# Kernel optimization log

Measured on AMD Instinct MI355X. Metric: run time of the kernel, lower is better.

## Reference

```python
import jax, jax.numpy as jnp
import numpy as np

B, C, H, W = 2, 512, 64, 64
HEADS, DHEAD = 8, 64
HID = HEADS * DHEAD  # 512
GROUPS = 32
EPS = 1e-5


def setup_inputs() -> dict:
    key = jax.random.key(0)
    ks = jax.random.split(key, 10)
    w_scale = 0.02
    return {
        "x": jax.random.normal(ks[0], (B, C, H, W), dtype=jnp.float32),
        "gamma": jnp.ones((C,), dtype=jnp.float32),
        "beta": jnp.zeros((C,), dtype=jnp.float32),
        "wq": jax.random.normal(ks[1], (HID, C), dtype=jnp.float32) * w_scale,
        "bq": jax.random.normal(ks[2], (HID,), dtype=jnp.float32) * w_scale,
        "wk": jax.random.normal(ks[3], (HID, C), dtype=jnp.float32) * w_scale,
        "bk": jax.random.normal(ks[4], (HID,), dtype=jnp.float32) * w_scale,
        "wv": jax.random.normal(ks[5], (HID, C), dtype=jnp.float32) * w_scale,
        "bv": jax.random.normal(ks[6], (HID,), dtype=jnp.float32) * w_scale,
        "wo": jax.random.normal(ks[7], (C, HID), dtype=jnp.float32) * w_scale,
        "bo": jax.random.normal(ks[8], (C,), dtype=jnp.float32) * w_scale,
    }


def _group_norm(x, gamma, beta):
    b, c, h, w = x.shape
    xg = x.reshape(b, GROUPS, c // GROUPS, h * w)
    mu = jnp.mean(xg, axis=(2, 3), keepdims=True)
    var = jnp.var(xg, axis=(2, 3), keepdims=True)
    xn = (xg - mu) * jax.lax.rsqrt(var + EPS)
    xn = xn.reshape(b, c, h, w)
    return xn * gamma[None, :, None, None] + beta[None, :, None, None]


def reference(x, gamma, beta, wq, bq, wk, bk, wv, bv, wo, bo):
    b, c, h, w = x.shape
    n = h * w
    # norm + flatten spatial; embedding=None -> self-attention on normed x
    xn = _group_norm(x, gamma, beta).reshape(b, c, n)
    # 1x1 Conv1d projections == channel matmuls
    q = jnp.einsum('oc,bcn->bon', wq, xn) + bq[None, :, None]
    k = jnp.einsum('oc,bcn->bon', wk, xn) + bk[None, :, None]
    v = jnp.einsum('oc,bcn->bon', wv, xn) + bv[None, :, None]
    scale = DHEAD ** (-0.25)  # applied to BOTH q and k, as in source
    qh = q.reshape(b, HEADS, DHEAD, n) * scale
    kh = k.reshape(b, HEADS, DHEAD, n) * scale
    vh = v.reshape(b, HEADS, DHEAD, n)
    # full NxN attention (the materialized score matrix targeted for kernel work)
    attn = jax.nn.softmax(jnp.einsum('bhdi,bhdj->bhij', qh, kh), axis=-1)
    out = jnp.einsum('bhij,bhdj->bhdi', attn, vh).reshape(b, HID, n)
    out = jnp.einsum('oc,bcn->bon', wo, out) + bo[None, :, None]
    out = out.reshape(b, c, h, w)
    return x + out  # in_channels == out_channels -> residual
```

## Files before the change

kernel.cpp:

```cpp
#include <hip/hip_runtime.h>
#include <math.h>

#define BB      2
#define CC      512
#define NN_TOK  4096
#define HEADS   8
#define DHEAD   64
#define HID     512
#define GROUPS  32
#define CPG     (CC / GROUPS)
#define EPS     1e-5f

typedef __bf16 bf16x8 __attribute__((ext_vector_type(8)));
typedef float  f32x4  __attribute__((ext_vector_type(4)));
typedef float  f32x16 __attribute__((ext_vector_type(16)));
typedef int    i32x8  __attribute__((ext_vector_type(8)));

static __device__ __forceinline__ unsigned short f2bf(float f) {
  __bf16 h = (__bf16)f;
  return __builtin_bit_cast(unsigned short, h);
}
static __device__ __forceinline__ float bf2f(unsigned short u) {
  unsigned v = (unsigned)u << 16;
  return __builtin_bit_cast(float, v);
}
static __device__ __forceinline__ unsigned pk_fp8x4(float a, float b, float c, float d) {
  int lo = __builtin_amdgcn_cvt_pk_fp8_f32(a, b, 0, false);
  return (unsigned)__builtin_amdgcn_cvt_pk_fp8_f32(c, d, lo, true);
}
static __device__ __forceinline__ unsigned char f2fp8(float a) {
  return (unsigned char)(__builtin_amdgcn_cvt_pk_fp8_f32(a, a, 0, false) & 0xff);
}
static __device__ __forceinline__ i32x8 ld_frag32(const unsigned char* p) {
  union { i32x8 v; long l[4]; } u;
  u.l[0] = *(const long*)(p + 0);
  u.l[1] = *(const long*)(p + 8);
  u.l[2] = *(const long*)(p + 16);
  u.l[3] = *(const long*)(p + 24);
  return u.v;
}
#define SC_ONE 0x7F7F7F7F
#define QKV_WS 32.0f
#define QKV_WS_INV 0.03125f
#define WO_WS 16.0f
#define WO_WS_INV 0.0625f

__global__ __launch_bounds__(256) void gn_stats_wconv_kernel(
    const float* __restrict__ x, float2* __restrict__ part,
    const float* __restrict__ wq, const float* __restrict__ wk,
    const float* __restrict__ wv, const float* __restrict__ wo,
    unsigned char* __restrict__ wq8, unsigned char* __restrict__ wk8,
    unsigned char* __restrict__ wv8, unsigned char* __restrict__ wo8) {
  int blk = blockIdx.x;
  int t = threadIdx.x;
  {
    int wsel = blk >> 6;
    int off = (blk & 63) * 4096 + t * 16;
    const float* s = (wsel == 0) ? wq : (wsel == 1) ? wk : (wsel == 2) ? wv : wo;
    unsigned char* d = (wsel == 0) ? wq8 : (wsel == 1) ? wk8 : (wsel == 2) ? wv8 : wo8;
    float sc = (wsel < 3) ? QKV_WS : WO_WS;
    #pragma unroll
    for (int i = 0; i < 4; ++i) {
      float4 a = *(const float4*)&s[off + i * 4];
      *(unsigned*)&d[off + i * 4] =
          pk_fp8x4(a.x * sc, a.y * sc, a.z * sc, a.w * sc);
    }
  }
  const float4* __restrict__ x4 = (const float4*)(x + (size_t)blk * 16384);
  float s = 0.f, ss = 0.f;
  #pragma unroll
  for (int i = 0; i < 16; ++i) {
    float4 v = x4[t + i * 256];
    s  += v.x + v.y + v.z + v.w;
    ss += v.x * v.x + v.y * v.y + v.z * v.z + v.w * v.w;
  }
  #pragma unroll
  for (int off = 32; off >= 1; off >>= 1) {
    s  += __shfl_down(s, off, 64);
    ss += __shfl_down(ss, off, 64);
  }
  __shared__ float rs[4], rss[4];
  int wid = t >> 6, lane = t & 63;
  if (lane == 0) { rs[wid] = s; rss[wid] = ss; }
  __syncthreads();
  if (t == 0) {
    float2 o;
    o.x = rs[0] + rs[1] + rs[2] + rs[3];
    o.y = rss[0] + rss[1] + rss[2] + rss[3];
    part[blk] = o;
  }
}

__global__ __launch_bounds__(256) void gn_norm_t_kernel(
    const float* __restrict__ x, const float* __restrict__ gamma,
    const float* __restrict__ beta, const float2* __restrict__ part,
    unsigned char* __restrict__ xnT8) {
  __shared__ __align__(16) unsigned short lds[64 * 72];
  __shared__ float mu4[4], rs4[4];
  int b = blockIdx.z;
  int t0 = blockIdx.x * 64, c0 = blockIdx.y * 64;
  int t = threadIdx.x;
  if (t < 4) {
    int g = (c0 >> 4) + t;
    int gi = b * GROUPS + g;
    float2 p0 = part[gi * 4 + 0], p1 = part[gi * 4 + 1];
    float2 p2 = part[gi * 4 + 2], p3 = part[gi * 4 + 3];
    float S = p0.x + p1.x + p2.x + p3.x;
    float SS = p0.y + p1.y + p2.y + p3.y;
    const float inv_n = 1.0f / (float)(CPG * NN_TOK);
    float mu = S * inv_n;
    float var = SS * inv_n - mu * mu;
    mu4[t] = mu;
    rs4[t] = rsqrtf(var + EPS);
  }
  __syncthreads();
  const float* __restrict__ xb = x + (size_t)b * CC * NN_TOK;
  #pragma unroll
  for (int i = 0; i < 4; ++i) {
    int f = t + i * 256;
    int row = f >> 4, c16 = f & 15;
    int c = c0 + row;
    float ga = gamma[c] * rs4[row >> 4];
    float be = beta[c] - mu4[row >> 4] * ga;
    float4 v = *(const float4*)&xb[(size_t)c * NN_TOK + t0 + c16 * 4];
    ushort4 pk;
    pk.x = f2bf(v.x * ga + be); pk.y = f2bf(v.y * ga + be);
    pk.z = f2bf(v.z * ga + be); pk.w = f2bf(v.w * ga + be);
    *(ushort4*)&lds[row * 72 + c16 * 4] = pk;
  }
  __syncthreads();
  unsigned char* __restrict__ ob = xnT8 + (size_t)b * NN_TOK * CC;
  #pragma unroll
  for (int i = 0; i < 2; ++i) {
    int f = t + i * 256;
    int row = f >> 3, ch = f & 7;
    float v0 = bf2f(lds[(ch * 8 + 0) * 72 + row]);
    float v1 = bf2f(lds[(ch * 8 + 1) * 72 + row]);
    float v2 = bf2f(lds[(ch * 8 + 2) * 72 + row]);
    float v3 = bf2f(lds[(ch * 8 + 3) * 72 + row]);
    float v4 = bf2f(lds[(ch * 8 + 4) * 72 + row]);
    float v5 = bf2f(lds[(ch * 8 + 5) * 72 + row]);
    float v6 = bf2f(lds[(ch * 8 + 6) * 72 + row]);
    float v7 = bf2f(lds[(ch * 8 + 7) * 72 + row]);
    unsigned lo = pk_fp8x4(v0, v1, v2, v3);
    unsigned hi = pk_fp8x4(v4, v5, v6, v7);
    *(uint2*)&ob[(size_t)(t0 + row) * CC + c0 + ch * 8] = make_uint2(lo, hi);
  }
}

__global__ __launch_bounds__(256, 3) void qkv_gemm_kernel(
    const unsigned char* __restrict__ xnT8,
    const unsigned char* __restrict__ wq8, const unsigned char* __restrict__ wk8,
    const unsigned char* __restrict__ wv8,
    const float* __restrict__ bq, const float* __restrict__ bk,
    const float* __restrict__ bv,
    unsigned char* __restrict__ qT8, unsigned char* __restrict__ kT8,
    unsigned char* __restrict__ vB8) {
  __shared__ __align__(16) unsigned char AB[2][2][128 * 72];
  int b = blockIdx.z;
  int y = blockIdx.y;
  int which = y >> 2, yl = y & 3;
  const unsigned char* __restrict__ W =
      (which == 0) ? wq8 : (which == 1) ? wk8 : wv8;
  const float* __restrict__ bias = (which == 0) ? bq : (which == 1) ? bk : bv;
  int m0 = yl * 128;
  int n0 = blockIdx.x * 128;
  const unsigned char* __restrict__ Bsrc = xnT8 + (size_t)b * NN_TOK * CC;
  int t = threadIdx.x, w = t >> 6, lane = t & 63;
  int wm = (w >> 1) * 64, wn = (w & 1) * 64;
  int l31 = lane & 31, q1h = lane >> 5;

  int sr0 = t >> 2, sr1 = (t + 256) >> 2, sch = t & 3;
  const unsigned char* Wa0 = &W[(size_t)(m0 + sr0) * CC + sch * 16];
  const unsigned char* Wa1 = &W[(size_t)(m0 + sr1) * CC + sch * 16];
  const unsigned char* Bb0 = &Bsrc[(size_t)(n0 + sr0) * CC + sch * 16];
  const unsigned char* Bb1 = &Bsrc[(size_t)(n0 + sr1) * CC + sch * 16];
  uint4 ra0 = *(const uint4*)(Wa0);
  uint4 ra1 = *(const uint4*)(Wa1);
  uint4 rb0 = *(const uint4*)(Bb0);
  uint4 rb1 = *(const uint4*)(Bb1);

  const f32x16 z16 = {0,0,0,0,0,0,0,0,0,0,0,0,0,0,0,0};
  f32x16 acc[2][2];
  #pragma unroll
  for (int mt = 0; mt < 2; ++mt)
    #pragma unroll
    for (int nt = 0; nt < 2; ++nt) acc[mt][nt] = z16;

  int cur = 0;
  for (int kc = 0; kc < CC; kc += 64) {
    __syncthreads();
    {
      unsigned char* As = AB[cur][0];
      unsigned char* Bs = AB[cur][1];
      unsigned char* ad0 = &As[sr0 * 72 + sch * 16];
      *(uint2*)ad0 = make_uint2(ra0.x, ra0.y);
      *(uint2*)(ad0 + 8) = make_uint2(ra0.z, ra0.w);
      unsigned char* ad1 = &As[sr1 * 72 + sch * 16];
      *(uint2*)ad1 = make_uint2(ra1.x, ra1.y);
      *(uint2*)(ad1 + 8) = make_uint2(ra1.z, ra1.w);
      unsigned char* bd0 = &Bs[sr0 * 72 + sch * 16];
      *(uint2*)bd0 = make_uint2(rb0.x, rb0.y);
      *(uint2*)(bd0 + 8) = make_uint2(rb0.z, rb0.w);
      unsigned char* bd1 = &Bs[sr1 * 72 + sch * 16];
      *(uint2*)bd1 = make_uint2(rb1.x, rb1.y);
      *(uint2*)(bd1 + 8) = make_uint2(rb1.z, rb1.w);
    }
    if (kc + 64 < CC) {
      ra0 = *(const uint4*)(Wa0 + kc + 64);
      ra1 = *(const uint4*)(Wa1 + kc + 64);
      rb0 = *(const uint4*)(Bb0 + kc + 64);
      rb1 = *(const uint4*)(Bb1 + kc + 64);
    }
    __syncthreads();
    const unsigned char* As = AB[cur][0];
    const unsigned char* Bs = AB[cur][1];
    i32x8 af[2], bfm[2];
    #pragma unroll
    for (int i = 0; i < 2; ++i) {
      af[i]  = ld_frag32(&As[(wm + i * 32 + l31) * 72 + q1h * 32]);
      bfm[i] = ld_frag32(&Bs[(wn + i * 32 + l31) * 72 + q1h * 32]);
    }
    #pragma unroll
    for (int mt = 0; mt < 2; ++mt)
      #pragma unroll
      for (int nt = 0; nt < 2; ++nt)
        acc[mt][nt] = __builtin_amdgcn_mfma_scale_f32_32x32x64_f8f6f4(
            af[mt], bfm[nt], acc[mt][nt], 0, 0, 0, SC_ONE, 0, SC_ONE);
    cur ^= 1;
  }
  __syncthreads();

  if (which < 2) {
    const float sc = (which == 0) ? 0.18033688011112043f : 1.0f;
    unsigned char* __restrict__ dstT = (which == 0) ? qT8 : kT8;
    unsigned char* buf = (unsigned char*)AB + w * 2560;
    int h = (m0 + wm) >> 6;
    const size_t hbase = (size_t)(b * HEADS + h) * NN_TOK;
    #pragma unroll
    for (int p = 0; p < 2; ++p) {
      #pragma unroll
      for (int mt = 0; mt < 2; ++mt) {
        #pragma unroll
        for (int g = 0; g < 4; ++g) {
          float4 bv4 = *(const float4*)&bias[m0 + wm + mt * 32 + g * 8 + q1h * 4];
          f32x16 a = acc[mt][p];
          unsigned pk = pk_fp8x4((a[4 * g + 0] * QKV_WS_INV + bv4.x) * sc,
                                 (a[4 * g + 1] * QKV_WS_INV + bv4.y) * sc,
                                 (a[4 * g + 2] * QKV_WS_INV + bv4.z) * sc,
                                 (a[4 * g + 3] * QKV_WS_INV + bv4.w) * sc);
          *(unsigned*)&buf[l31 * 80 + mt * 32 + g * 8 + q1h * 4] = pk;
        }
      }
      #pragma unroll
      for (int it = 0; it < 2; ++it) {
        int idx = it * 64 + lane;
        int row = idx >> 2, ch = idx & 3;
        int tok = n0 + wn + p * 32 + row;
        *(uint4*)&dstT[(hbase + tok) * DHEAD + ch * 16] =
            *(const uint4*)&buf[row * 80 + ch * 16];
      }
      __syncthreads();
    }
  } else {
    unsigned char* __restrict__ dst = vB8 + (size_t)b * HID * NN_TOK;
    #pragma unroll
    for (int mt = 0; mt < 2; ++mt) {
      #pragma unroll
      for (int g = 0; g < 4; ++g) {
        float4 bv4 = *(const float4*)&bias[m0 + wm + mt * 32 + g * 8 + q1h * 4];
        float bvr[4] = {bv4.x, bv4.y, bv4.z, bv4.w};
        #pragma unroll
        for (int nt = 0; nt < 2; ++nt) {
          int tok = n0 + wn + nt * 32 + l31;
          #pragma unroll
          for (int r = 0; r < 4; ++r) {
            int m = m0 + wm + mt * 32 + g * 8 + q1h * 4 + r;
            dst[(size_t)m * NN_TOK + tok] =
                f2fp8(acc[mt][nt][4 * g + r] * QKV_WS_INV + bvr[r]);
          }
        }
      }
    }
  }
}

__global__ __launch_bounds__(256) void outproj_kernel(
    const unsigned char* __restrict__ aoT8, const unsigned char* __restrict__ wo8,
    const float* __restrict__ bo, const float* __restrict__ x,
    float* __restrict__ out) {
  __shared__ __align__(16) unsigned char As8[2][128 * 80];
  __shared__ __align__(16) unsigned char Bs8[2][64 * 80];
  int b = blockIdx.z;
  int m0 = blockIdx.y * 128;
  int n0 = blockIdx.x * 64;
  const unsigned char* __restrict__ Bsrc = aoT8 + (size_t)b * NN_TOK * HID;
  int t = threadIdx.x, w = t >> 6, lane = t & 63;
  int wm = (w & 1) * 64, wn = (w >> 1) * 32;
  int l31 = lane & 31, q1h = lane >> 5;

  int ar0 = t >> 2, ar1 = (t + 256) >> 2, ach = t & 3;
  const unsigned char* pa0 = &wo8[(size_t)(m0 + ar0) * HID + ach * 16];
  const unsigned char* pa1 = &wo8[(size_t)(m0 + ar1) * HID + ach * 16];
  const unsigned char* pb  = &Bsrc[(size_t)(n0 + ar0) * HID + ach * 16];
  uint4 ra0 = *(const uint4*)(pa0);
  uint4 ra1 = *(const uint4*)(pa1);
  uint4 rb  = *(const uint4*)(pb);

  const f32x16 z16 = {0,0,0,0,0,0,0,0,0,0,0,0,0,0,0,0};
  f32x16 acc[2];
  acc[0] = z16; acc[1] = z16;

  int cur = 0;
  for (int kc = 0; kc < HID; kc += 64) {
    __syncthreads();
    *(uint4*)&As8[cur][ar0 * 80 + ach * 16] = ra0;
    *(uint4*)&As8[cur][ar1 * 80 + ach * 16] = ra1;
    *(uint4*)&Bs8[cur][ar0 * 80 + ach * 16] = rb;
    if (kc + 64 < HID) {
      ra0 = *(const uint4*)(pa0 + kc + 64);
      ra1 = *(const uint4*)(pa1 + kc + 64);
      rb  = *(const uint4*)(pb + kc + 64);
    }
    __syncthreads();
    i32x8 bfm = ld_frag32(&Bs8[cur][(wn + l31) * 80 + q1h * 32]);
    #pragma unroll
    for (int mt = 0; mt < 2; ++mt) {
      i32x8 af = ld_frag32(&As8[cur][(wm + mt * 32 + l31) * 80 + q1h * 32]);
      acc[mt] = __builtin_amdgcn_mfma_scale_f32_32x32x64_f8f6f4(
          af, bfm, acc[mt], 0, 0, 0, SC_ONE, 0, SC_ONE);
    }
    cur ^= 1;
  }

  const float* __restrict__ xb = x + (size_t)b * CC * NN_TOK;
  float* __restrict__ ob = out + (size_t)b * CC * NN_TOK;
  int tok = n0 + wn + l31;
  #pragma unroll
  for (int mt = 0; mt < 2; ++mt) {
    #pragma unroll
    for (int g = 0; g < 4; ++g) {
      float4 bv4 = *(const float4*)&bo[m0 + wm + mt * 32 + g * 8 + q1h * 4];
      float bvr[4] = {bv4.x, bv4.y, bv4.z, bv4.w};
      #pragma unroll
      for (int r = 0; r < 4; ++r) {
        int m = m0 + wm + mt * 32 + g * 8 + q1h * 4 + r;
        size_t off = (size_t)m * NN_TOK + tok;
        ob[off] = acc[mt][4 * g + r] * WO_WS_INV + bvr[r] + xb[off];
      }
    }
  }
}

__global__ __launch_bounds__(512, 4) void attn_mfma_kernel(
    const unsigned char* __restrict__ qT8, const unsigned char* __restrict__ kT8,
    const unsigned char* __restrict__ vv8, unsigned char* __restrict__ aoT8) {
  __shared__ __align__(16) unsigned char kvs[2 * 18432];
  __shared__ __align__(16) unsigned char st8[4 * 32 * 80];
  __shared__ float lbuf[128];
  int bh = blockIdx.y;
  int b = bh >> 3, h = bh & 7;
  int i0 = blockIdx.x * 128;
  const size_t hb = (size_t)bh * NN_TOK;
  const unsigned char* __restrict__ qtg = qT8 + hb * DHEAD;
  const unsigned char* __restrict__ ktg = kT8 + hb * DHEAD;
  const unsigned char* __restrict__ vg  = vv8 + hb * DHEAD;
  int t = threadIdx.x;
  int w = t >> 6, lane = t & 63, l31 = lane & 31, q1h = lane >> 5;
  int strip = w & 3, parity = w >> 2;
  int iw = i0 + strip * 32;

  const unsigned char* qrow = qtg + (size_t)(iw + l31) * DHEAD + q1h * 32;
  uint4 qv0 = *(const uint4*)(qrow);
  uint4 qv1 = *(const uint4*)(qrow + 16);
  i32x8 qf = {(int)qv0.x, (int)qv0.y, (int)qv0.z, (int)qv0.w,
              (int)qv1.x, (int)qv1.y, (int)qv1.z, (int)qv1.w};
  i32x8 ones;
  #pragma unroll
  for (int i = 0; i < 8; ++i) ones[i] = 0x38383838;

  int jr = t >> 2, ch = t & 3;
  int ktile = jr >> 6, krow = jr & 63;
  int vtile = t >> 8, vrr = (t >> 2) & 63, vch = t & 3;
  const unsigned char* kga = &ktg[(size_t)jr * DHEAD + ch * 16];
  const unsigned char* vga = &vg[(size_t)vrr * NN_TOK + vtile * 64 + vch * 16];
  int kldso = ktile * 4608 + krow * 72 + ch * 16;
  int vldso = 9216 + vtile * 4608 + vrr * 72 + vch * 16;

  uint4 kx = *(const uint4*)(kga);
  uint4 vx = *(const uint4*)(vga);

  const f32x16 z16 = {0,0,0,0,0,0,0,0,0,0,0,0,0,0,0,0};
  f32x16 o0 = z16, o1 = z16, lacc = z16;

  int cur = 0;
  for (int rt = 0; rt < NN_TOK / 128; ++rt) {
    __syncthreads();
    unsigned char* kb = kvs + cur * 18432;
    {
      unsigned char* kd = kb + kldso;
      *(uint2*)kd = make_uint2(kx.x, kx.y);
      *(uint2*)(kd + 8) = make_uint2(kx.z, kx.w);
      unsigned char* vd = kb + vldso;
      *(uint2*)vd = make_uint2(vx.x, vx.y);
      *(uint2*)(vd + 8) = make_uint2(vx.z, vx.w);
    }
    if (rt + 1 < NN_TOK / 128) {
      kx = *(const uint4*)(kga + (size_t)(rt + 1) * 128 * DHEAD);
      vx = *(const uint4*)(vga + (rt + 1) * 128);
    }
    __syncthreads();
    const unsigned char* ksw = kb + parity * 4608;
    const unsigned char* vsw = kb + 9216 + parity * 4608;

    i32x8 ka0 = ld_frag32(&ksw[l31 * 72 + q1h * 32]);
    i32x8 ka1 = ld_frag32(&ksw[(32 + l31) * 72 + q1h * 32]);
    f32x16 s0 = __builtin_amdgcn_mfma_scale_f32_32x32x64_f8f6f4(
        ka0, qf, z16, 0, 0, 0, SC_ONE, 0, SC_ONE);
    f32x16 s1 = __builtin_amdgcn_mfma_scale_f32_32x32x64_f8f6f4(
        ka1, qf, z16, 0, 0, 0, SC_ONE, 0, SC_ONE);

    unsigned pk4[8];
    #pragma unroll
    for (int g = 0; g < 4; ++g) {
      float p0 = __builtin_amdgcn_exp2f(s0[4 * g + 0]);
      float p1 = __builtin_amdgcn_exp2f(s0[4 * g + 1]);
      float p2 = __builtin_amdgcn_exp2f(s0[4 * g + 2]);
      float p3 = __builtin_amdgcn_exp2f(s0[4 * g + 3]);
      pk4[g] = pk_fp8x4(p0, p1, p2, p3);
    }
    #pragma unroll
    for (int g = 0; g < 4; ++g) {
      float p0 = __builtin_amdgcn_exp2f(s1[4 * g + 0]);
      float p1 = __builtin_amdgcn_exp2f(s1[4 * g + 1]);
      float p2 = __builtin_amdgcn_exp2f(s1[4 * g + 2]);
      float p3 = __builtin_amdgcn_exp2f(s1[4 * g + 3]);
      pk4[4 + g] = pk_fp8x4(p0, p1, p2, p3);
    }

    i32x8 pb;
    #pragma unroll
    for (int g = 0; g < 4; ++g) {
      unsigned send = q1h ? pk4[g] : pk4[4 + g];
      unsigned got = (unsigned)__shfl_xor((int)send, 32);
      pb[2 * g]     = (int)(q1h ? got : pk4[g]);
      pb[2 * g + 1] = (int)(q1h ? pk4[4 + g] : got);
    }

    i32x8 va0 = ld_frag32(&vsw[l31 * 72 + q1h * 32]);
    i32x8 va1 = ld_frag32(&vsw[(32 + l31) * 72 + q1h * 32]);
    o0 = __builtin_amdgcn_mfma_scale_f32_32x32x64_f8f6f4(
        va0, pb, o0, 0, 0, 0, SC_ONE, 0, SC_ONE);
    o1 = __builtin_amdgcn_mfma_scale_f32_32x32x64_f8f6f4(
        va1, pb, o1, 0, 0, 0, SC_ONE, 0, SC_ONE);
    lacc = __builtin_amdgcn_mfma_scale_f32_32x32x64_f8f6f4(
        ones, pb, lacc, 0, 0, 0, SC_ONE, 0, SC_ONE);
    cur ^= 1;
  }
  float lrun = lacc[0];

  float* obuf = (float*)kvs;
  __syncthreads();
  if (parity == 1) {
    #pragma unroll
    for (int r = 0; r < 16; ++r) {
      int d = (r & 3) + 8 * (r >> 2) + 4 * q1h;
      obuf[strip * 1024 + d * 32 + l31] = o0[r];
    }
    if (q1h == 0) lbuf[strip * 32 + l31] = lrun;
  }
  __syncthreads();
  if (parity == 0) {
    lrun += lbuf[strip * 32 + l31];
    #pragma unroll
    for (int r = 0; r < 16; ++r) {
      int d = (r & 3) + 8 * (r >> 2) + 4 * q1h;
      o0[r] += obuf[strip * 1024 + d * 32 + l31];
    }
  }
  __syncthreads();
  if (parity == 1) {
    #pragma unroll
    for (int r = 0; r < 16; ++r) {
      int d = (r & 3) + 8 * (r >> 2) + 4 * q1h;
      obuf[strip * 1024 + d * 32 + l31] = o1[r];
    }
  }
  __syncthreads();
  if (parity == 0) {
    #pragma unroll
    for (int r = 0; r < 16; ++r) {
      int d = (r & 3) + 8 * (r >> 2) + 4 * q1h;
      o1[r] += obuf[strip * 1024 + d * 32 + l31];
    }
    float inv = 1.0f / lrun;
    unsigned char* stw = st8 + strip * 2560;
    #pragma unroll
    for (int dm = 0; dm < 2; ++dm) {
      #pragma unroll
      for (int g = 0; g < 4; ++g) {
        float v0 = ((dm == 0) ? o0[4 * g + 0] : o1[4 * g + 0]) * inv;
        float v1 = ((dm == 0) ? o0[4 * g + 1] : o1[4 * g + 1]) * inv;
        float v2 = ((dm == 0) ? o0[4 * g + 2] : o1[4 * g + 2]) * inv;
        float v3 = ((dm == 0) ? o0[4 * g + 3] : o1[4 * g + 3]) * inv;
        *(unsigned*)&stw[l31 * 80 + dm * 32 + g * 8 + q1h * 4] =
            pk_fp8x4(v0, v1, v2, v3);
      }
    }
    const size_t obase = (size_t)b * NN_TOK;
    #pragma unroll
    for (int it = 0; it < 4; ++it) {
      int idx = it * 64 + lane;
      int row = idx >> 3, ch = idx & 7;
      int tok = iw + row;
      *(uint2*)&aoT8[(obase + tok) * HID + h * DHEAD + ch * 8] =
          *(const uint2*)&stw[row * 80 + ch * 8];
    }
  }
}

extern "C" void kernel_launch(void* const* d_in, const int* in_sizes, int n_in,
                              void* d_out, int out_size, void* d_ws, size_t ws_size,
                              hipStream_t stream) {
  const float* x     = (const float*)d_in[0];
  const float* gamma = (const float*)d_in[1];
  const float* beta  = (const float*)d_in[2];
  const float* wq    = (const float*)d_in[3];
  const float* bq    = (const float*)d_in[4];
  const float* wk    = (const float*)d_in[5];
  const float* bk    = (const float*)d_in[6];
  const float* wv    = (const float*)d_in[7];
  const float* bv    = (const float*)d_in[8];
  const float* wo    = (const float*)d_in[9];
  const float* bo    = (const float*)d_in[10];
  float* out = (float*)d_out;

  const size_t SZ = (size_t)BB * CC * NN_TOK;
  const size_t WZ = (size_t)CC * HID;
  unsigned char* xnT8 = (unsigned char*)d_ws;
  unsigned char* qT8  = xnT8 + SZ;
  unsigned char* kT8  = qT8 + SZ;
  unsigned char* vB8  = kT8 + SZ;
  unsigned char* aoT8 = vB8 + SZ;
  unsigned char* wq8  = aoT8 + SZ;
  unsigned char* wk8  = wq8 + WZ;
  unsigned char* wv8  = wk8 + WZ;
  unsigned char* wo8  = wv8 + WZ;
  float2* gnpart = (float2*)(wo8 + WZ);

  gn_stats_wconv_kernel<<<dim3(256), dim3(256), 0, stream>>>(
      x, gnpart, wq, wk, wv, wo, wq8, wk8, wv8, wo8);

  gn_norm_t_kernel<<<dim3(NN_TOK / 64, CC / 64, BB), dim3(256), 0, stream>>>(
      x, gamma, beta, gnpart, xnT8);

  qkv_gemm_kernel<<<dim3(NN_TOK / 128, 12, BB), dim3(256), 0, stream>>>(
      xnT8, wq8, wk8, wv8, bq, bk, bv, qT8, kT8, vB8);

  attn_mfma_kernel<<<dim3(NN_TOK / 128, BB * HEADS), dim3(512), 0, stream>>>(
      qT8, kT8, vB8, aoT8);

  outproj_kernel<<<dim3(NN_TOK / 64, CC / 128, BB), dim3(256), 0, stream>>>(
      aoT8, wo8, bo, x, out);
}
```

Baseline: 176.1 us.

## Load K/V MFMA fragments directly from global memory, dropping LDS staging

The attention loop no longer stages K and V tiles through double-buffered shared memory with two block barriers per iteration. Each wave now reads its own K and V fragments straight from global memory (via L1/L2) into registers. This removes the LDS writes, the LDS reads and the __syncthreads in the hot loop, and shrinks shared memory, which may allow more resident blocks. In exchange, the four waves of a block sharing a parity each fetch the same K/V data, global load latency is no longer hidden by register prefetch, and the V loads are strided by NN_TOK.

```diff
diff --git a/kernel.cpp b/kernel.cpp
--- a/kernel.cpp
+++ b/kernel.cpp
@@ -37,6 +37,12 @@
   u.l[1] = *(const long*)(p + 8);
   u.l[2] = *(const long*)(p + 16);
   u.l[3] = *(const long*)(p + 24);
+  return u.v;
+}
+static __device__ __forceinline__ i32x8 ld_g32(const unsigned char* p) {
+  union { i32x8 v; uint4 q[2]; } u;
+  u.q[0] = *(const uint4*)(p);
+  u.q[1] = *(const uint4*)(p + 16);
   return u.v;
 }
 #define SC_ONE 0x7F7F7F7F
@@ -355,7 +361,7 @@
 __global__ __launch_bounds__(512, 4) void attn_mfma_kernel(
     const unsigned char* __restrict__ qT8, const unsigned char* __restrict__ kT8,
     const unsigned char* __restrict__ vv8, unsigned char* __restrict__ aoT8) {
-  __shared__ __align__(16) unsigned char kvs[2 * 18432];
+  __shared__ float obuf[4 * 1024];
   __shared__ __align__(16) unsigned char st8[4 * 32 * 80];
   __shared__ float lbuf[128];
   int bh = blockIdx.y;
@@ -379,42 +385,16 @@
   #pragma unroll
   for (int i = 0; i < 8; ++i) ones[i] = 0x38383838;
 
-  int jr = t >> 2, ch = t & 3;
-  int ktile = jr >> 6, krow = jr & 63;
-  int vtile = t >> 8, vrr = (t >> 2) & 63, vch = t & 3;
-  const unsigned char* kga = &ktg[(size_t)jr * DHEAD + ch * 16];
-  const unsigned char* vga = &vg[(size_t)vrr * NN_TOK + vtile * 64 + vch * 16];
-  int kldso = ktile * 4608 + krow * 72 + ch * 16;
-  int vldso = 9216 + vtile * 4608 + vrr * 72 + vch * 16;
-
-  uint4 kx = *(const uint4*)(kga);
-  uint4 vx = *(const uint4*)(vga);
-
   const f32x16 z16 = {0,0,0,0,0,0,0,0,0,0,0,0,0,0,0,0};
   f32x16 o0 = z16, o1 = z16, lacc = z16;
 
-  int cur = 0;
+  const unsigned char* kfb = ktg + (size_t)(parity * 64 + l31) * DHEAD + q1h * 32;
+  const unsigned char* vfb = vg + (size_t)l31 * NN_TOK + parity * 64 + q1h * 32;
+
   for (int rt = 0; rt < NN_TOK / 128; ++rt) {
-    __syncthreads();
-    unsigned char* kb = kvs + cur * 18432;
-    {
-      unsigned char* kd = kb + kldso;
-      *(uint2*)kd = make_uint2(kx.x, kx.y);
-      *(uint2*)(kd + 8) = make_uint2(kx.z, kx.w);
-      unsigned char* vd = kb + vldso;
-      *(uint2*)vd = make_uint2(vx.x, vx.y);
-      *(uint2*)(vd + 8) = make_uint2(vx.z, vx.w);
-    }
-    if (rt + 1 < NN_TOK / 128) {
-      kx = *(const uint4*)(kga + (size_t)(rt + 1) * 128 * DHEAD);
-      vx = *(const uint4*)(vga + (rt + 1) * 128);
-    }
-    __syncthreads();
-    const unsigned char* ksw = kb + parity * 4608;
-    const unsigned char* vsw = kb + 9216 + parity * 4608;
-
-    i32x8 ka0 = ld_frag32(&ksw[l31 * 72 + q1h * 32]);
-    i32x8 ka1 = ld_frag32(&ksw[(32 + l31) * 72 + q1h * 32]);
+    int j0 = rt * 128;
+    i32x8 ka0 = ld_g32(kfb + (size_t)j0 * DHEAD);
+    i32x8 ka1 = ld_g32(kfb + (size_t)(j0 + 32) * DHEAD);
     f32x16 s0 = __builtin_amdgcn_mfma_scale_f32_32x32x64_f8f6f4(
         ka0, qf, z16, 0, 0, 0, SC_ONE, 0, SC_ONE);
     f32x16 s1 = __builtin_amdgcn_mfma_scale_f32_32x32x64_f8f6f4(
@@ -447,19 +427,17 @@
       pb[2 * g + 1] = (int)(q1h ? pk4[4 + g] : got);
     }
 
-    i32x8 va0 = ld_frag32(&vsw[l31 * 72 + q1h * 32]);
-    i32x8 va1 = ld_frag32(&vsw[(32 + l31) * 72 + q1h * 32]);
+    i32x8 va0 = ld_g32(vfb + j0);
+    i32x8 va1 = ld_g32(vfb + (size_t)32 * NN_TOK + j0);
     o0 = __builtin_amdgcn_mfma_scale_f32_32x32x64_f8f6f4(
         va0, pb, o0, 0, 0, 0, SC_ONE, 0, SC_ONE);
     o1 = __builtin_amdgcn_mfma_scale_f32_32x32x64_f8f6f4(
         va1, pb, o1, 0, 0, 0, SC_ONE, 0, SC_ONE);
     lacc = __builtin_amdgcn_mfma_scale_f32_32x32x64_f8f6f4(
         ones, pb, lacc, 0, 0, 0, SC_ONE, 0, SC_ONE);
-    cur ^= 1;
   }
   float lrun = lacc[0];
 
-  float* obuf = (float*)kvs;
   __syncthreads();
   if (parity == 1) {
     #pragma unroll
```

Result: slower. 208.7 us (+18.5%).
